# Kernel optimization log

Hardware: AMD Instinct MI355X
Metric: run time of the kernel (lower is better)

## Reference

```python
import jax, jax.numpy as jnp
import numpy as np

PIXEL_SIZE = 0.1
PI = 3.141592653589793


def setup_inputs() -> dict:
    key = jax.random.key(0)
    batch = jax.random.normal(key, (128, 1, 512, 512), dtype=jnp.float32)
    return {"batch": batch}


def _hann_window(roi):
    # lin = linspace(-roi/2, roi/2, roi); r[i,j] = sqrt(lin[j]^2 + lin[i]^2)
    lin = jnp.linspace(-roi / 2, roi / 2, roi, dtype=jnp.float32)
    r = jnp.sqrt(lin[None, :] ** 2 + lin[:, None] ** 2)
    hann = 0.5 * (1.0 + jnp.cos(PI * r / (roi / 2)))
    hann = jnp.where(r > roi / 2, 0.0, hann)
    return hann  # [roi, roi]


def _radial_segments(roi, n_freq):
    # radialDst = round(sqrt(xx^2 + yy^2)) with x = arange(-cx, roi-cx)
    cx = roi // 2
    x = np.arange(-cx, roi - cx, dtype=np.float64)
    xx, yy = np.meshgrid(x, x, indexing="ij")
    rad = np.round(np.sqrt(xx ** 2 + yy ** 2)).astype(np.int32)
    # bins >= n_freq go into an overflow segment that is discarded
    seg = np.where(rad < n_freq, rad, n_freq)
    return jnp.asarray(seg.ravel())


def reference(batch):
    px = PIXEL_SIZE
    roi = batch.shape[-1]
    cx = roi // 2
    n_freq = cx + 1
    nyquist = 1.0 / (2.0 * px)

    # subtract per-ROI mean
    batch_nm = batch - jnp.mean(batch, axis=(2, 3), keepdims=True)

    # Hann-windowed 2D power spectrum, averaged over realizations
    hann = _hann_window(roi)[None, None, :, :]
    F = jnp.fft.fftshift(jnp.fft.fft2(batch_nm * hann, axes=(2, 3)), axes=(2, 3))
    ps = jnp.mean(jnp.abs(F) ** 2, axis=0)            # [1, roi, roi]
    nps2D = (px ** 2 / roi ** 2) * jnp.squeeze(ps)    # [roi, roi]

    # single-pass radial mean binning (replaces per-k boolean-mask loop)
    seg = _radial_segments(roi, n_freq)
    flat = nps2D.ravel()
    sums = jax.ops.segment_sum(flat, seg, num_segments=n_freq + 1)[:n_freq]
    counts = jax.ops.segment_sum(jnp.ones_like(flat), seg, num_segments=n_freq + 1)[:n_freq]
    nps1D = sums / counts

    f1D = jnp.linspace(0.0, nyquist, n_freq, dtype=jnp.float32)
    return nps1D, nps2D, f1D
```

## Files before the change

### kernel.cpp

```cpp
#include <hip/hip_runtime.h>
#include <hip/hip_fp16.h>

#define N 512
#define NF 257
#define NB 128
#define PI_F 3.14159265358979323846f
#define C_SQ2 0.70710678118654752440f

__device__ __forceinline__ float2 cmul(float2 a, float2 b) {
    return make_float2(a.x * b.x - a.y * b.y, a.x * b.y + a.y * b.x);
}
__device__ __forceinline__ void bf(float2& a, float2& b) {
    float2 t = b;
    b = make_float2(a.x - t.x, a.y - t.y);
    a = make_float2(a.x + t.x, a.y + t.y);
}
__device__ __forceinline__ void bf_tw(float2& a, float2& b, float2 w) {
    float2 t = cmul(b, w);
    b = make_float2(a.x - t.x, a.y - t.y);
    a = make_float2(a.x + t.x, a.y + t.y);
}
__device__ __forceinline__ void bf_ni(float2& a, float2& b) {
    float2 t = make_float2(b.y, -b.x);
    b = make_float2(a.x - t.x, a.y - t.y);
    a = make_float2(a.x + t.x, a.y + t.y);
}
__device__ __forceinline__ void lds_order() {
    asm volatile("" ::: "memory");
}

__device__ __forceinline__ void fft512_core(float2 v[8], float2* st, int l) {
    const float2 w64  = make_float2(C_SQ2, -C_SQ2);
    const float2 w192 = make_float2(-C_SQ2, -C_SQ2);
    lds_order();
    bf(v[0], v[1]); bf(v[2], v[3]); bf(v[4], v[5]); bf(v[6], v[7]);
    bf(v[0], v[2]); bf_ni(v[1], v[3]); bf(v[4], v[6]); bf_ni(v[5], v[7]);
    bf(v[0], v[4]); bf_tw(v[1], v[5], w64); bf_ni(v[2], v[6]); bf_tw(v[3], v[7], w192);
#pragma unroll
    for (int e = 0; e < 8; e++) st[9 * l + e] = v[e];
    lds_order();
    int g = l >> 3, r = l & 7;
#pragma unroll
    for (int t = 0; t < 8; t++) v[t] = st[72 * g + 9 * t + r];
    float sn, cs;
    __sincosf(-(PI_F / 32.0f) * (float)r, &sn, &cs);
    float2 W1 = make_float2(cs, sn);
    float2 W2 = cmul(W1, W1);
    float2 W3 = cmul(W2, W2);
    float2 W2n = make_float2(W2.y, -W2.x);
    bf_tw(v[0], v[1], W3); bf_tw(v[2], v[3], W3); bf_tw(v[4], v[5], W3); bf_tw(v[6], v[7], W3);
    bf_tw(v[0], v[2], W2); bf_tw(v[1], v[3], W2n); bf_tw(v[4], v[6], W2); bf_tw(v[5], v[7], W2n);
    {
        float2 W1a = cmul(W1, w64);
        float2 W1n = make_float2(W1.y, -W1.x);
        float2 W1c = cmul(W1, w192);
        bf_tw(v[0], v[4], W1); bf_tw(v[1], v[5], W1a); bf_tw(v[2], v[6], W1n); bf_tw(v[3], v[7], W1c);
    }
    lds_order();
#pragma unroll
    for (int t = 0; t < 8; t++) st[72 * g + 9 * t + r] = v[t];
    lds_order();
#pragma unroll
    for (int t = 0; t < 8; t++) v[t] = st[72 * t + l + (l >> 3)];
    __sincosf(-(PI_F / 256.0f) * (float)l, &sn, &cs);
    float2 Wc = make_float2(cs, sn);
    float2 w2 = cmul(Wc, Wc);
    float2 w4 = cmul(w2, w2);
    float2 w2n = make_float2(w2.y, -w2.x);
    bf_tw(v[0], v[1], w4); bf_tw(v[2], v[3], w4); bf_tw(v[4], v[5], w4); bf_tw(v[6], v[7], w4);
    bf_tw(v[0], v[2], w2); bf_tw(v[1], v[3], w2n); bf_tw(v[4], v[6], w2); bf_tw(v[5], v[7], w2n);
    {
        float2 Wca = cmul(Wc, w64);
        float2 Wcn = make_float2(Wc.y, -Wc.x);
        float2 Wcc = cmul(Wc, w192);
        bf_tw(v[0], v[4], Wc); bf_tw(v[1], v[5], Wca); bf_tw(v[2], v[6], Wcn); bf_tw(v[3], v[7], Wcc);
    }
}

__global__ void zero_kernel(float* __restrict__ accH, float* __restrict__ bins,
                            float* __restrict__ meanacc) {
    int i = blockIdx.x * blockDim.x + threadIdx.x;
    if (i < NF * N) accH[i] = 0.0f;
    if (i < 2 * (NF + 1)) bins[i] = 0.0f;
    if (i < NB) meanacc[i] = 0.0f;
}

__global__ __launch_bounds__(256) void hanntab_kernel(float* __restrict__ htab) {
    int i = blockIdx.x * 256 + threadIdx.x;
    int r = i >> 9, c = i & (N - 1);
    const float step = (float)N / (float)(N - 1);
    float a = -0.5f * (float)N + (float)r * step;
    float b = -0.5f * (float)N + (float)c * step;
    float rr = sqrtf(a * a + b * b);
    float h = (rr > 256.0f) ? 0.0f : 0.5f * (1.0f + cosf(rr * (PI_F / 256.0f)));
    htab[i] = h;
}

__global__ __launch_bounds__(512) void hannfft_kernel(const float* __restrict__ htab,
                                                      float2* __restrict__ Hrow) {
    __shared__ float sm[9216];
    int tid = threadIdx.x;
    int w = tid >> 6, l = tid & 63;
    int rowbase = blockIdx.x << 4;
    int r1 = rowbase + 2 * w;
    int rl = __brev((unsigned)l) >> 26;
    const int bre[8] = {0, 4, 2, 6, 1, 5, 3, 7};
    const float* h1 = htab + (size_t)r1 * N + rl;
    const float* h2 = h1 + N;

    float2 v[8];
#pragma unroll
    for (int e = 0; e < 8; e++) {
        int o = bre[e] << 6;
        v[e] = make_float2(h1[o], h2[o]);
    }

    float2* st = (float2*)sm + w * 576;
    fft512_core(v, st, l);
    __syncthreads();

    float* tre = sm;
    float* tim = sm + 4240;
    int lr0 = 2 * w, lr1 = lr0 + 1;
    int sl = (64 - l) & 63;
#pragma unroll
    for (int t = 0; t <= 4; t++) {
        float2 a = v[7 - t];
        float zfx = __shfl(a.x, sl);
        float zfy = __shfl(a.y, sl);
        if (l == 0) { float2 o = v[(8 - t) & 7]; zfx = o.x; zfy = o.y; }
        float2 z = v[t];
        int col = 64 * t + l;
        if (col < NF) {
            tre[lr0 * 265 + col] = 0.5f * (z.x + zfx);
            tim[lr0 * 265 + col] = 0.5f * (z.y - zfy);
            tre[lr1 * 265 + col] = 0.5f * (z.y + zfy);
            tim[lr1 * 265 + col] = 0.5f * (zfx - z.x);
        }
    }
    __syncthreads();

    int c0 = tid >> 4, rr = tid & 15;
#pragma unroll
    for (int it = 0; it < 9; it++) {
        int c = it * 32 + c0;
        if (c < NF) {
            float2 val = make_float2(tre[rr * 265 + c], tim[rr * 265 + c]);
            Hrow[(size_t)c * N + rowbase + rr] = val;
        }
    }
}

__global__ __launch_bounds__(512, 4) void rowfft_kernel(const float* __restrict__ x,
                                                        const float* __restrict__ htab,
                                                        float* __restrict__ meanacc,
                                                        __half2* __restrict__ inter) {
    __shared__ float sm[9216];
    __shared__ float redsum[8];
    int tid = threadIdx.x;
    int w = tid >> 6, l = tid & 63;
    int img = blockIdx.x >> 5;
    int rowbase = (blockIdx.x & 31) << 4;
    int r1 = rowbase + 2 * w;
    int rl = __brev((unsigned)l) >> 26;
    const int bre[8] = {0, 4, 2, 6, 1, 5, 3, 7};
    const float* xr1 = x + ((size_t)img * N + r1) * N + rl;
    const float* xr2 = xr1 + N;
    const float* hr1 = htab + (size_t)r1 * N + rl;
    const float* hr2 = hr1 + N;

    float a1[8], a2[8], b1[8], b2[8];
#pragma unroll
    for (int e = 0; e < 8; e++) {
        int o = bre[e] << 6;
        a1[e] = xr1[o]; a2[e] = xr2[o];
        b1[e] = hr1[o]; b2[e] = hr2[o];
    }

    float rsum = 0.0f;
#pragma unroll
    for (int e = 0; e < 8; e++) rsum += a1[e] + a2[e];

    float2 v[8];
#pragma unroll
    for (int e = 0; e < 8; e++) v[e] = make_float2(a1[e] * b1[e], a2[e] * b2[e]);

#pragma unroll
    for (int off = 32; off > 0; off >>= 1) rsum += __shfl_down(rsum, off);
    if (l == 0) redsum[w] = rsum;

    float2* st = (float2*)sm + w * 576;
    fft512_core(v, st, l);
    __syncthreads();
    if (tid == 0) {
        float s = 0.0f;
#pragma unroll
        for (int i = 0; i < 8; i++) s += redsum[i];
        atomicAdd(meanacc + img, s);
    }

    __half2* tile = (__half2*)sm;
    int lr0 = 2 * w, lr1 = lr0 + 1;
    int sl = (64 - l) & 63;
#pragma unroll
    for (int t = 0; t <= 4; t++) {
        float2 a = v[7 - t];
        float zfx = __shfl(a.x, sl);
        float zfy = __shfl(a.y, sl);
        if (l == 0) { float2 o = v[(8 - t) & 7]; zfx = o.x; zfy = o.y; }
        float2 z = v[t];
        int col = 64 * t + l;
        if (col < NF) {
            tile[lr0 * 265 + col] = __floats2half2_rn(0.5f * (z.x + zfx), 0.5f * (z.y - zfy));
            tile[lr1 * 265 + col] = __floats2half2_rn(0.5f * (z.y + zfy), 0.5f * (zfx - z.x));
        }
    }
    __syncthreads();

    int c0 = tid >> 4, rr = tid & 15;
#pragma unroll
    for (int it = 0; it < 9; it++) {
        int c = it * 32 + c0;
        if (c < NF) {
            inter[((size_t)img * NF + c) * N + rowbase + rr] = tile[rr * 265 + c];
        }
    }
}

__global__ __launch_bounds__(256, 4) void colfft_kernel(const __half2* __restrict__ inter,
                                                        const float2* __restrict__ Hrow,
                                                        const float* __restrict__ meanacc,
                                                        float* __restrict__ accH) {
    __shared__ float sm[4608];
    int tid = threadIdx.x;
    int w = tid >> 6, l = tid & 63;
    int col = blockIdx.x * 4 + w;
    int colc = col < NF ? col : NF - 1;
    int b0 = blockIdx.y * 8;
    float2* st = (float2*)sm + w * 576;
    int rl = __brev((unsigned)l) >> 26;
    const int bre[8] = {0, 4, 2, 6, 1, 5, 3, 7};

    float2 hc[8];
    const float2* hp = Hrow + (size_t)colc * N + rl;
#pragma unroll
    for (int e = 0; e < 8; e++) hc[e] = hp[bre[e] << 6];

    float mn8[8];
#pragma unroll
    for (int bi = 0; bi < 8; bi++)
        mn8[bi] = meanacc[b0 + bi] * (1.0f / ((float)N * (float)N));

    float pw[8];
#pragma unroll
    for (int t = 0; t < 8; t++) pw[t] = 0.0f;

    __half2 cur[8], nxt[8];
    const __half2* ip0 = inter + ((size_t)b0 * NF + colc) * N + rl;
#pragma unroll
    for (int e = 0; e < 8; e++) cur[e] = ip0[bre[e] << 6];

    for (int bi = 0; bi < 8; bi++) {
        if (bi < 7) {
            const __half2* np = inter + ((size_t)(b0 + bi + 1) * NF + colc) * N + rl;
#pragma unroll
            for (int e = 0; e < 8; e++) nxt[e] = np[bre[e] << 6];
        }
        float mn = mn8[bi];
        float2 v[8];
#pragma unroll
        for (int e = 0; e < 8; e++) {
            float2 z = __half22float2(cur[e]);
            v[e] = make_float2(z.x - mn * hc[e].x, z.y - mn * hc[e].y);
        }
        fft512_core(v, st, l);
#pragma unroll
        for (int t = 0; t < 8; t++)
            pw[t] += v[t].x * v[t].x + v[t].y * v[t].y;
#pragma unroll
        for (int e = 0; e < 8; e++) cur[e] = nxt[e];
    }

    if (col < NF) {
#pragma unroll
        for (int t = 0; t < 8; t++)
            atomicAdd(&accH[(size_t)col * N + 64 * t + l], pw[t]);
    }
}

__global__ __launch_bounds__(256) void finalize2d_kernel(const float* __restrict__ accH,
                                                         float* __restrict__ out2d,
                                                         float* __restrict__ bins) {
    __shared__ float lsum[NF];
    __shared__ float lcnt[NF];
    int t = threadIdx.x;
    for (int i = t; i < NF; i += 256) { lsum[i] = 0.0f; lcnt[i] = 0.0f; }
    __syncthreads();
    const float scale = (0.1f * 0.1f) / ((float)N * (float)N) / (float)NB;
    int idx = blockIdx.x * 256 + t;
    int stride = gridDim.x * 256;
    for (int p = idx; p < N * N; p += stride) {
        int i = p >> 9, j = p & (N - 1);
        int jm = (j + 256) & 511;
        int col, k;
        if (jm < NF) { col = jm; k = (i + 256) & 511; }
        else         { col = 256 - j; k = (256 - i) & 511; }
        float v = accH[((size_t)col << 9) + k] * scale;
        out2d[p] = v;
        float xi = (float)(i - 256), yj = (float)(j - 256);
        int rad = (int)rintf(sqrtf(xi * xi + yj * yj));
        if (rad < NF) { atomicAdd(&lsum[rad], v); atomicAdd(&lcnt[rad], 1.0f); }
    }
    __syncthreads();
    for (int i = t; i < NF; i += 256) {
        if (lsum[i] != 0.0f || lcnt[i] != 0.0f) {
            atomicAdd(&bins[i], lsum[i]);
            atomicAdd(&bins[NF + 1 + i], lcnt[i]);
        }
    }
}

__global__ void finalize1d_kernel(const float* __restrict__ bins, float* __restrict__ out) {
    int t = blockIdx.x * blockDim.x + threadIdx.x;
    if (t < NF) {
        out[t] = bins[t] / bins[NF + 1 + t];
        out[NF + N * N + t] = (float)t * (5.0f / 256.0f);
    }
}

extern "C" void kernel_launch(void* const* d_in, const int* in_sizes, int n_in,
                              void* d_out, int out_size, void* d_ws, size_t ws_size,
                              hipStream_t stream) {
    const float* x = (const float*)d_in[0];
    float* out = (float*)d_out;
    char* ws = (char*)d_ws;

    float* accH    = (float*)ws;
    float* meanacc = (float*)(ws + (size_t)NF * N * sizeof(float));
    float* bins    = meanacc + NB;
    size_t off_h = (size_t)NF * N * sizeof(float) + NB * sizeof(float)
                   + 2 * (NF + 1) * sizeof(float);
    off_h = (off_h + 255) & ~(size_t)255;
    float2* Hrow = (float2*)(ws + off_h);
    size_t off_t = off_h + (size_t)NF * N * sizeof(float2);
    off_t = (off_t + 255) & ~(size_t)255;
    float* htab = (float*)(ws + off_t);
    size_t off_inter = off_t + (size_t)N * N * sizeof(float);
    off_inter = (off_inter + 255) & ~(size_t)255;
    __half2* inter = (__half2*)(ws + off_inter);

    zero_kernel<<<dim3((NF * N + 255) / 256), dim3(256), 0, stream>>>(accH, bins, meanacc);
    hanntab_kernel<<<dim3(N * N / 256), dim3(256), 0, stream>>>(htab);
    hannfft_kernel<<<dim3(32), dim3(512), 0, stream>>>(htab, Hrow);
    rowfft_kernel<<<dim3(NB * 32), dim3(512), 0, stream>>>(x, htab, meanacc, inter);
    colfft_kernel<<<dim3(65, 16), dim3(256), 0, stream>>>(inter, Hrow, meanacc, accH);
    finalize2d_kernel<<<dim3(256), dim3(256), 0, stream>>>(accH, out + NF, bins);
    finalize1d_kernel<<<dim3(2), dim3(256), 0, stream>>>(bins, out);
}
```

Before: 265.3 us.

## Interleave two 512-point FFTs per wave in row and column kernels

Adds a dual-FFT routine that runs two independent 512-point FFTs per wavefront, interleaving their butterfly phases and sharing twiddle computation. The row kernel now handles four rows per wave (32 rows per block, half the blocks). The column kernel processes two images per pass over 4 images per block instead of 8 sequentially, doubling grid y. This is meant to raise instruction-level parallelism and hide LDS and global latency, at the cost of higher register pressure that may reduce occupancy. The row kernel's LDS tile also grows to 32 rows, so it has to fit within the existing shared array.

```diff
diff --git a/kernel.cpp b/kernel.cpp
--- a/kernel.cpp
+++ b/kernel.cpp
@@ -29,17 +29,30 @@
     asm volatile("" ::: "memory");
 }
 
+__device__ __forceinline__ void fft_phaseA(float2 v[8]) {
+    const float2 w64  = make_float2(C_SQ2, -C_SQ2);
+    const float2 w192 = make_float2(-C_SQ2, -C_SQ2);
+    bf(v[0], v[1]); bf(v[2], v[3]); bf(v[4], v[5]); bf(v[6], v[7]);
+    bf(v[0], v[2]); bf_ni(v[1], v[3]); bf(v[4], v[6]); bf_ni(v[5], v[7]);
+    bf(v[0], v[4]); bf_tw(v[1], v[5], w64); bf_ni(v[2], v[6]); bf_tw(v[3], v[7], w192);
+}
+__device__ __forceinline__ void fft_phaseBC(float2 v[8], float2 W1, float2 W1a,
+                                            float2 W1n, float2 W1c, float2 W2,
+                                            float2 W2n, float2 W3) {
+    bf_tw(v[0], v[1], W3); bf_tw(v[2], v[3], W3); bf_tw(v[4], v[5], W3); bf_tw(v[6], v[7], W3);
+    bf_tw(v[0], v[2], W2); bf_tw(v[1], v[3], W2n); bf_tw(v[4], v[6], W2); bf_tw(v[5], v[7], W2n);
+    bf_tw(v[0], v[4], W1); bf_tw(v[1], v[5], W1a); bf_tw(v[2], v[6], W1n); bf_tw(v[3], v[7], W1c);
+}
+
 __device__ __forceinline__ void fft512_core(float2 v[8], float2* st, int l) {
     const float2 w64  = make_float2(C_SQ2, -C_SQ2);
     const float2 w192 = make_float2(-C_SQ2, -C_SQ2);
-    lds_order();
-    bf(v[0], v[1]); bf(v[2], v[3]); bf(v[4], v[5]); bf(v[6], v[7]);
-    bf(v[0], v[2]); bf_ni(v[1], v[3]); bf(v[4], v[6]); bf_ni(v[5], v[7]);
-    bf(v[0], v[4]); bf_tw(v[1], v[5], w64); bf_ni(v[2], v[6]); bf_tw(v[3], v[7], w192);
+    int g = l >> 3, r = l & 7;
+    lds_order();
+    fft_phaseA(v);
 #pragma unroll
     for (int e = 0; e < 8; e++) st[9 * l + e] = v[e];
     lds_order();
-    int g = l >> 3, r = l & 7;
 #pragma unroll
     for (int t = 0; t < 8; t++) v[t] = st[72 * g + 9 * t + r];
     float sn, cs;
@@ -48,14 +61,10 @@
     float2 W2 = cmul(W1, W1);
     float2 W3 = cmul(W2, W2);
     float2 W2n = make_float2(W2.y, -W2.x);
-    bf_tw(v[0], v[1], W3); bf_tw(v[2], v[3], W3); bf_tw(v[4], v[5], W3); bf_tw(v[6], v[7], W3);
-    bf_tw(v[0], v[2], W2); bf_tw(v[1], v[3], W2n); bf_tw(v[4], v[6], W2); bf_tw(v[5], v[7], W2n);
-    {
-        float2 W1a = cmul(W1, w64);
-        float2 W1n = make_float2(W1.y, -W1.x);
-        float2 W1c = cmul(W1, w192);
-        bf_tw(v[0], v[4], W1); bf_tw(v[1], v[5], W1a); bf_tw(v[2], v[6], W1n); bf_tw(v[3], v[7], W1c);
-    }
+    float2 W1a = cmul(W1, w64);
+    float2 W1n = make_float2(W1.y, -W1.x);
+    float2 W1c = cmul(W1, w192);
+    fft_phaseBC(v, W1, W1a, W1n, W1c, W2, W2n, W3);
     lds_order();
 #pragma unroll
     for (int t = 0; t < 8; t++) st[72 * g + 9 * t + r] = v[t];
@@ -67,13 +76,78 @@
     float2 w2 = cmul(Wc, Wc);
     float2 w4 = cmul(w2, w2);
     float2 w2n = make_float2(w2.y, -w2.x);
-    bf_tw(v[0], v[1], w4); bf_tw(v[2], v[3], w4); bf_tw(v[4], v[5], w4); bf_tw(v[6], v[7], w4);
-    bf_tw(v[0], v[2], w2); bf_tw(v[1], v[3], w2n); bf_tw(v[4], v[6], w2); bf_tw(v[5], v[7], w2n);
-    {
-        float2 Wca = cmul(Wc, w64);
-        float2 Wcn = make_float2(Wc.y, -Wc.x);
-        float2 Wcc = cmul(Wc, w192);
-        bf_tw(v[0], v[4], Wc); bf_tw(v[1], v[5], Wca); bf_tw(v[2], v[6], Wcn); bf_tw(v[3], v[7], Wcc);
+    float2 Wca = cmul(Wc, w64);
+    float2 Wcn = make_float2(Wc.y, -Wc.x);
+    float2 Wcc = cmul(Wc, w192);
+    fft_phaseBC(v, Wc, Wca, Wcn, Wcc, w2, w2n, w4);
+}
+
+__device__ __forceinline__ void fft512_x2(float2 va[8], float2 vb[8], float2* st, int l) {
+    const float2 w64  = make_float2(C_SQ2, -C_SQ2);
+    const float2 w192 = make_float2(-C_SQ2, -C_SQ2);
+    int g = l >> 3, r = l & 7;
+    fft_phaseA(va); fft_phaseA(vb);
+    lds_order();
+#pragma unroll
+    for (int e = 0; e < 8; e++) st[9 * l + e] = va[e];
+    lds_order();
+#pragma unroll
+    for (int t = 0; t < 8; t++) va[t] = st[72 * g + 9 * t + r];
+    lds_order();
+#pragma unroll
+    for (int e = 0; e < 8; e++) st[9 * l + e] = vb[e];
+    lds_order();
+#pragma unroll
+    for (int t = 0; t < 8; t++) vb[t] = st[72 * g + 9 * t + r];
+    float sn, cs;
+    __sincosf(-(PI_F / 32.0f) * (float)r, &sn, &cs);
+    float2 W1 = make_float2(cs, sn);
+    float2 W2 = cmul(W1, W1);
+    float2 W3 = cmul(W2, W2);
+    float2 W2n = make_float2(W2.y, -W2.x);
+    float2 W1a = cmul(W1, w64);
+    float2 W1n = make_float2(W1.y, -W1.x);
+    float2 W1c = cmul(W1, w192);
+    fft_phaseBC(va, W1, W1a, W1n, W1c, W2, W2n, W3);
+    fft_phaseBC(vb, W1, W1a, W1n, W1c, W2, W2n, W3);
+    lds_order();
+#pragma unroll
+    for (int t = 0; t < 8; t++) st[72 * g + 9 * t + r] = va[t];
+    lds_order();
+#pragma unroll
+    for (int t = 0; t < 8; t++) va[t] = st[72 * t + l + (l >> 3)];
+    lds_order();
+#pragma unroll
+    for (int t = 0; t < 8; t++) st[72 * g + 9 * t + r] = vb[t];
+    lds_order();
+#pragma unroll
+    for (int t = 0; t < 8; t++) vb[t] = st[72 * t + l + (l >> 3)];
+    __sincosf(-(PI_F / 256.0f) * (float)l, &sn, &cs);
+    float2 Wc = make_float2(cs, sn);
+    float2 w2 = cmul(Wc, Wc);
+    float2 w4 = cmul(w2, w2);
+    float2 w2n = make_float2(w2.y, -w2.x);
+    float2 Wca = cmul(Wc, w64);
+    float2 Wcn = make_float2(Wc.y, -Wc.x);
+    float2 Wcc = cmul(Wc, w192);
+    fft_phaseBC(va, Wc, Wca, Wcn, Wcc, w2, w2n, w4);
+    fft_phaseBC(vb, Wc, Wca, Wcn, Wcc, w2, w2n, w4);
+}
+
+__device__ __forceinline__ void unpack_rows(const float2 v[8], __half2* tile,
+                                            int lr0, int lr1, int l, int sl) {
+#pragma unroll
+    for (int t = 0; t <= 4; t++) {
+        float2 a = v[7 - t];
+        float zfx = __shfl(a.x, sl);
+        float zfy = __shfl(a.y, sl);
+        if (l == 0) { float2 o = v[(8 - t) & 7]; zfx = o.x; zfy = o.y; }
+        float2 z = v[t];
+        int col = 64 * t + l;
+        if (col < NF) {
+            tile[lr0 * 265 + col] = __floats2half2_rn(0.5f * (z.x + zfx), 0.5f * (z.y - zfy));
+            tile[lr1 * 265 + col] = __floats2half2_rn(0.5f * (z.y + zfy), 0.5f * (zfx - z.x));
+        }
     }
 }
 
@@ -159,38 +233,44 @@
     __shared__ float redsum[8];
     int tid = threadIdx.x;
     int w = tid >> 6, l = tid & 63;
-    int img = blockIdx.x >> 5;
-    int rowbase = (blockIdx.x & 31) << 4;
-    int r1 = rowbase + 2 * w;
+    int img = blockIdx.x >> 4;
+    int rowbase = (blockIdx.x & 15) << 5;
+    int r1 = rowbase + 4 * w;
     int rl = __brev((unsigned)l) >> 26;
     const int bre[8] = {0, 4, 2, 6, 1, 5, 3, 7};
-    const float* xr1 = x + ((size_t)img * N + r1) * N + rl;
-    const float* xr2 = xr1 + N;
-    const float* hr1 = htab + (size_t)r1 * N + rl;
-    const float* hr2 = hr1 + N;
-
-    float a1[8], a2[8], b1[8], b2[8];
+    const float* xp = x + ((size_t)img * N + r1) * N + rl;
+    const float* hp = htab + (size_t)r1 * N + rl;
+
+    float ax[4][8], hx[4][8];
+#pragma unroll
+    for (int j = 0; j < 4; j++)
+#pragma unroll
+        for (int e = 0; e < 8; e++) ax[j][e] = xp[j * N + (bre[e] << 6)];
+#pragma unroll
+    for (int j = 0; j < 4; j++)
+#pragma unroll
+        for (int e = 0; e < 8; e++) hx[j][e] = hp[j * N + (bre[e] << 6)];
+    __builtin_amdgcn_sched_barrier(0);
+
+    float rsum = 0.0f;
+#pragma unroll
+    for (int j = 0; j < 4; j++)
+#pragma unroll
+        for (int e = 0; e < 8; e++) rsum += ax[j][e];
+
+    float2 va[8], vb[8];
 #pragma unroll
     for (int e = 0; e < 8; e++) {
-        int o = bre[e] << 6;
-        a1[e] = xr1[o]; a2[e] = xr2[o];
-        b1[e] = hr1[o]; b2[e] = hr2[o];
-    }
-
-    float rsum = 0.0f;
-#pragma unroll
-    for (int e = 0; e < 8; e++) rsum += a1[e] + a2[e];
-
-    float2 v[8];
-#pragma unroll
-    for (int e = 0; e < 8; e++) v[e] = make_float2(a1[e] * b1[e], a2[e] * b2[e]);
+        va[e] = make_float2(ax[0][e] * hx[0][e], ax[1][e] * hx[1][e]);
+        vb[e] = make_float2(ax[2][e] * hx[2][e], ax[3][e] * hx[3][e]);
+    }
 
 #pragma unroll
     for (int off = 32; off > 0; off >>= 1) rsum += __shfl_down(rsum, off);
     if (l == 0) redsum[w] = rsum;
 
     float2* st = (float2*)sm + w * 576;
-    fft512_core(v, st, l);
+    fft512_x2(va, vb, st, l);
     __syncthreads();
     if (tid == 0) {
         float s = 0.0f;
@@ -200,27 +280,15 @@
     }
 
     __half2* tile = (__half2*)sm;
-    int lr0 = 2 * w, lr1 = lr0 + 1;
     int sl = (64 - l) & 63;
-#pragma unroll
-    for (int t = 0; t <= 4; t++) {
-        float2 a = v[7 - t];
-        float zfx = __shfl(a.x, sl);
-        float zfy = __shfl(a.y, sl);
-        if (l == 0) { float2 o = v[(8 - t) & 7]; zfx = o.x; zfy = o.y; }
-        float2 z = v[t];
-        int col = 64 * t + l;
-        if (col < NF) {
-            tile[lr0 * 265 + col] = __floats2half2_rn(0.5f * (z.x + zfx), 0.5f * (z.y - zfy));
-            tile[lr1 * 265 + col] = __floats2half2_rn(0.5f * (z.y + zfy), 0.5f * (zfx - z.x));
-        }
-    }
-    __syncthreads();
-
-    int c0 = tid >> 4, rr = tid & 15;
-#pragma unroll
-    for (int it = 0; it < 9; it++) {
-        int c = it * 32 + c0;
+    unpack_rows(va, tile, 4 * w, 4 * w + 1, l, sl);
+    unpack_rows(vb, tile, 4 * w + 2, 4 * w + 3, l, sl);
+    __syncthreads();
+
+    int c0 = tid >> 5, rr = tid & 31;
+#pragma unroll
+    for (int it = 0; it < 17; it++) {
+        int c = it * 16 + c0;
         if (c < NF) {
             inter[((size_t)img * NF + c) * N + rowbase + rr] = tile[rr * 265 + c];
         }
@@ -236,7 +304,7 @@
     int w = tid >> 6, l = tid & 63;
     int col = blockIdx.x * 4 + w;
     int colc = col < NF ? col : NF - 1;
-    int b0 = blockIdx.y * 8;
+    int b0 = blockIdx.y * 4;
     float2* st = (float2*)sm + w * 576;
     int rl = __brev((unsigned)l) >> 26;
     const int bre[8] = {0, 4, 2, 6, 1, 5, 3, 7};
@@ -246,39 +314,51 @@
 #pragma unroll
     for (int e = 0; e < 8; e++) hc[e] = hp[bre[e] << 6];
 
-    float mn8[8];
-#pragma unroll
-    for (int bi = 0; bi < 8; bi++)
-        mn8[bi] = meanacc[b0 + bi] * (1.0f / ((float)N * (float)N));
+    float mn[4];
+#pragma unroll
+    for (int i = 0; i < 4; i++)
+        mn[i] = meanacc[b0 + i] * (1.0f / ((float)N * (float)N));
 
     float pw[8];
 #pragma unroll
     for (int t = 0; t < 8; t++) pw[t] = 0.0f;
 
-    __half2 cur[8], nxt[8];
-    const __half2* ip0 = inter + ((size_t)b0 * NF + colc) * N + rl;
-#pragma unroll
-    for (int e = 0; e < 8; e++) cur[e] = ip0[bre[e] << 6];
-
-    for (int bi = 0; bi < 8; bi++) {
-        if (bi < 7) {
-            const __half2* np = inter + ((size_t)(b0 + bi + 1) * NF + colc) * N + rl;
-#pragma unroll
-            for (int e = 0; e < 8; e++) nxt[e] = np[bre[e] << 6];
-        }
-        float mn = mn8[bi];
-        float2 v[8];
+    const size_t istr = (size_t)NF * N;
+    const __half2* base = inter + ((size_t)b0 * NF + colc) * N + rl;
+
+    __half2 cA[8], cB[8], nA[8], nB[8];
+#pragma unroll
+    for (int e = 0; e < 8; e++) {
+        cA[e] = base[bre[e] << 6];
+        cB[e] = base[istr + (bre[e] << 6)];
+    }
+    __builtin_amdgcn_sched_barrier(0);
+
+#pragma unroll
+    for (int it = 0; it < 2; it++) {
+        if (it == 0) {
+#pragma unroll
+            for (int e = 0; e < 8; e++) {
+                nA[e] = base[2 * istr + (bre[e] << 6)];
+                nB[e] = base[3 * istr + (bre[e] << 6)];
+            }
+        }
+        float mA = mn[2 * it], mB = mn[2 * it + 1];
+        float2 va[8], vb[8];
 #pragma unroll
         for (int e = 0; e < 8; e++) {
-            float2 z = __half22float2(cur[e]);
-            v[e] = make_float2(z.x - mn * hc[e].x, z.y - mn * hc[e].y);
-        }
-        fft512_core(v, st, l);
+            float2 zA = __half22float2(cA[e]);
+            float2 zB = __half22float2(cB[e]);
+            va[e] = make_float2(zA.x - mA * hc[e].x, zA.y - mA * hc[e].y);
+            vb[e] = make_float2(zB.x - mB * hc[e].x, zB.y - mB * hc[e].y);
+        }
+        fft512_x2(va, vb, st, l);
 #pragma unroll
         for (int t = 0; t < 8; t++)
-            pw[t] += v[t].x * v[t].x + v[t].y * v[t].y;
-#pragma unroll
-        for (int e = 0; e < 8; e++) cur[e] = nxt[e];
+            pw[t] += va[t].x * va[t].x + va[t].y * va[t].y
+                   + vb[t].x * vb[t].x + vb[t].y * vb[t].y;
+#pragma unroll
+        for (int e = 0; e < 8; e++) { cA[e] = nA[e]; cB[e] = nB[e]; }
     }
 
     if (col < NF) {
@@ -352,8 +432,8 @@
     zero_kernel<<<dim3((NF * N + 255) / 256), dim3(256), 0, stream>>>(accH, bins, meanacc);
     hanntab_kernel<<<dim3(N * N / 256), dim3(256), 0, stream>>>(htab);
     hannfft_kernel<<<dim3(32), dim3(512), 0, stream>>>(htab, Hrow);
-    rowfft_kernel<<<dim3(NB * 32), dim3(512), 0, stream>>>(x, htab, meanacc, inter);
-    colfft_kernel<<<dim3(65, 16), dim3(256), 0, stream>>>(inter, Hrow, meanacc, accH);
+    rowfft_kernel<<<dim3(NB * 16), dim3(512), 0, stream>>>(x, htab, meanacc, inter);
+    colfft_kernel<<<dim3(65, 32), dim3(256), 0, stream>>>(inter, Hrow, meanacc, accH);
     finalize2d_kernel<<<dim3(256), dim3(256), 0, stream>>>(accH, out + NF, bins);
     finalize1d_kernel<<<dim3(2), dim3(256), 0, stream>>>(bins, out);
 }
```

Measured after the change: 256.1 us. -3.5%, faster.
